# Kernel tuning notes

Measured on AMD Instinct MI355X. Metric: run time of the kernel, lower is better.

## Reference

```python
import jax, jax.numpy as jnp
import numpy as np

N_NODES = 100000
N_EDGES = 625000
D = 128
DEPTH = 2
BN_EPS = 1e-5


def setup_inputs() -> dict:
    key = jax.random.key(0)
    ks = jax.random.split(key, 8)
    x = jax.random.normal(ks[0], (N_NODES, D), dtype=jnp.float32)
    edge_index = jax.random.randint(ks[1], (2, N_EDGES), 0, N_NODES, dtype=jnp.int64)
    edge_weight = jax.random.uniform(ks[2], (N_EDGES,), dtype=jnp.float32)
    s = 1.0 / np.sqrt(D)
    W_lin = jax.random.uniform(ks[3], (DEPTH, D, D), jnp.float32, -s, s)
    W_gcn = jax.random.uniform(ks[4], (DEPTH, D, D), jnp.float32, -s, s)
    gamma = jnp.ones((DEPTH, D), jnp.float32)
    beta = jnp.zeros((DEPTH, D), jnp.float32)
    return {"x": x, "edge_index": edge_index, "edge_weight": edge_weight,
            "W_lin": W_lin, "W_gcn": W_gcn, "gamma": gamma, "beta": beta}


def reference(x, edge_index, edge_weight, W_lin, W_gcn, gamma, beta):
    n = x.shape[0]
    row, col = edge_index[0], edge_index[1]  # source, target
    # gcn_norm with add_self_loops=False: deg over targets, symmetric normalization
    deg = jax.ops.segment_sum(edge_weight, col, num_segments=n)
    dinv = jnp.where(deg > 0, jax.lax.rsqrt(deg), 0.0)
    norm = dinv[row] * edge_weight * dinv[col]  # [E]

    for i in range(DEPTH):
        hl = x @ W_lin[i].T                       # parallel linear branch
        hg = x @ W_gcn[i].T                       # GCNConv linear
        msg = norm[:, None] * hg[row]             # [E, D] messages
        hr = jax.ops.segment_sum(msg, col, num_segments=n)
        h = hl + hr
        # BatchNorm1d, training mode (batch statistics, biased variance)
        mu = jnp.mean(h, axis=0)
        var = jnp.mean((h - mu) ** 2, axis=0)
        h = (h - mu) * jax.lax.rsqrt(var + BN_EPS) * gamma[i] + beta[i]
        x = jnp.maximum(h, 0.0) if i != DEPTH - 1 else h
    return x
```

## Files before the change

kernel.cpp:

```cpp
#include <hip/hip_runtime.h>

#define NN 100000
#define NE 625000
#define DD 128
#define CAP 32
#define NREP 8

#define CONVB 12500
#define WPACKB 256
#define FILLBLK ((NE + 255) / 256)
#define GB ((NN + 63) / 64)

typedef __attribute__((ext_vector_type(8))) short bf16x8;
typedef __attribute__((ext_vector_type(4))) float f32x4;

static __device__ __forceinline__ unsigned short f2bf(float f) {
    union { float f; unsigned u; } v; v.f = f;
    unsigned u = v.u + 0x7fffu + ((v.u >> 16) & 1u);
    return (unsigned short)(u >> 16);
}
static __device__ __forceinline__ float bflo(unsigned u) { return __uint_as_float(u << 16); }
static __device__ __forceinline__ float bfhi(unsigned u) { return __uint_as_float(u & 0xffff0000u); }

__global__ __launch_bounds__(256) void k_pre(const float* __restrict__ x,
                                             unsigned* __restrict__ Xb2,
                                             const float* __restrict__ Wl,
                                             const float* __restrict__ Wg,
                                             unsigned short* __restrict__ wp,
                                             const int* __restrict__ row,
                                             const int* __restrict__ col,
                                             const float* __restrict__ w,
                                             int* __restrict__ cnt,
                                             int2* __restrict__ ebuf) {
    int b = blockIdx.x, t = threadIdx.x;
    if (b < CONVB) {
        size_t i = (size_t)b * 256 + t;
        size_t base = i * 4;
        float4 v = *(const float4*)&x[base];
        uint2 o;
        o.x = (unsigned)f2bf(v.x) | ((unsigned)f2bf(v.y) << 16);
        o.y = (unsigned)f2bf(v.z) | ((unsigned)f2bf(v.w) << 16);
        *(uint2*)&Xb2[i * 2] = o;
    } else if (b < CONVB + WPACKB) {
        int idx = (b - CONVB) * 256 + t;
        int l = idx >> 15;
        int rem = idx & 32767;
        int n = rem >> 8;
        int k = rem & 255;
        float v = (k < 128) ? Wl[(size_t)l * DD * DD + n * DD + k]
                            : Wg[(size_t)l * DD * DD + n * DD + (k - 128)];
        int wv = n >> 5;
        int tt = (n >> 4) & 1;
        int i  = n & 15;
        int ss = k >> 5;
        int q  = (k >> 3) & 3;
        int j  = k & 7;
        size_t off = ((size_t)((((l * 4 + wv) * 2 + tt) * 8 + ss)) * 64 + q * 16 + i) * 8 + j;
        wp[off] = f2bf(v);
    } else {
        int e = (b - CONVB - WPACKB) * 256 + t;
        if (e < NE) {
            int r = row[e], c = col[e];
            int pos = atomicAdd(&cnt[c], 1);
            if (pos < CAP) {
                int2 v; v.x = r; v.y = __float_as_int(w[e]);
                ebuf[(size_t)c * CAP + pos] = v;
            }
        }
    }
}

__global__ __launch_bounds__(256) void k_dinvb(const int* __restrict__ cnt,
                                               const int2* __restrict__ ebuf,
                                               float* __restrict__ dinv) {
    int t = threadIdx.x;
    int node = blockIdx.x * 32 + (t >> 3);
    int l = t & 7;
    int c = cnt[node]; if (c > CAP) c = CAP;
    float s = 0.f;
    for (int p = l; p < c; p += 8) s += __int_as_float(ebuf[(size_t)node * CAP + p].y);
    s += __shfl_down(s, 4, 8);
    s += __shfl_down(s, 2, 8);
    s += __shfl_down(s, 1, 8);
    if (l == 0) dinv[node] = (s > 0.f) ? rsqrtf(s) : 0.f;
}

template<int BN>
__global__ __launch_bounds__(256) void k_gatherP(const int* __restrict__ cnt,
                                                 const int2* __restrict__ ebuf,
                                                 const float* __restrict__ dinv,
                                                 const unsigned* __restrict__ X2,
                                                 const float* __restrict__ scale,
                                                 const float* __restrict__ shift,
                                                 unsigned* __restrict__ P2) {
    int t = threadIdx.x;
    int node = blockIdx.x * 4 + (t >> 6);
    int lane = t & 63;
    int c = cnt[node]; if (c > CAP) c = CAP;
    const int2* eb = ebuf + (size_t)node * CAP;
    float dn = dinv[node];
    float scx = 0.f, scy = 0.f, shx = 0.f, shy = 0.f;
    if (BN) {
        scx = scale[2 * lane]; scy = scale[2 * lane + 1];
        shx = shift[2 * lane]; shy = shift[2 * lane + 1];
    }
    float ax = 0.f, ay = 0.f;
    int p = 0;
    for (; p + 3 < c; p += 4) {
        int2 e0 = eb[p], e1 = eb[p + 1], e2 = eb[p + 2], e3 = eb[p + 3];
        float w0 = __int_as_float(e0.y) * dinv[e0.x] * dn;
        float w1 = __int_as_float(e1.y) * dinv[e1.x] * dn;
        float w2 = __int_as_float(e2.y) * dinv[e2.x] * dn;
        float w3 = __int_as_float(e3.y) * dinv[e3.x] * dn;
        unsigned u0 = X2[(size_t)e0.x * 64 + lane];
        unsigned u1 = X2[(size_t)e1.x * 64 + lane];
        unsigned u2 = X2[(size_t)e2.x * 64 + lane];
        unsigned u3 = X2[(size_t)e3.x * 64 + lane];
        float x0 = bflo(u0), y0 = bfhi(u0);
        float x1 = bflo(u1), y1 = bfhi(u1);
        float x2 = bflo(u2), y2 = bfhi(u2);
        float x3 = bflo(u3), y3 = bfhi(u3);
        if (BN) {
            x0 = fmaxf(x0 * scx + shx, 0.f); y0 = fmaxf(y0 * scy + shy, 0.f);
            x1 = fmaxf(x1 * scx + shx, 0.f); y1 = fmaxf(y1 * scy + shy, 0.f);
            x2 = fmaxf(x2 * scx + shx, 0.f); y2 = fmaxf(y2 * scy + shy, 0.f);
            x3 = fmaxf(x3 * scx + shx, 0.f); y3 = fmaxf(y3 * scy + shy, 0.f);
        }
        ax += w0 * x0 + w1 * x1 + w2 * x2 + w3 * x3;
        ay += w0 * y0 + w1 * y1 + w2 * y2 + w3 * y3;
    }
    for (; p < c; p++) {
        int2 e0 = eb[p];
        float w0 = __int_as_float(e0.y) * dinv[e0.x] * dn;
        unsigned u0 = X2[(size_t)e0.x * 64 + lane];
        float x0 = bflo(u0), y0 = bfhi(u0);
        if (BN) {
            x0 = fmaxf(x0 * scx + shx, 0.f); y0 = fmaxf(y0 * scy + shy, 0.f);
        }
        ax += w0 * x0;
        ay += w0 * y0;
    }
    P2[(size_t)node * 64 + lane] = (unsigned)f2bf(ax) | ((unsigned)f2bf(ay) << 16);
}

template<int LAYER>
__global__ __launch_bounds__(256) void k_gemm_s(const unsigned short* Xin,
                                                const unsigned short* P,
                                                const unsigned short* __restrict__ wp,
                                                const float* __restrict__ scale,
                                                const float* __restrict__ shift,
                                                unsigned short* Hout,
                                                float* __restrict__ stats) {
    __shared__ __align__(16) char smem[33792];
    unsigned short* sAv = (unsigned short*)smem;
    unsigned short* sBv = (unsigned short*)smem;
    float* red = (float*)(smem + 17408);

    const int t = threadIdx.x;
    const int wave = t >> 6;
    const int lane = t & 63;
    const int i16 = lane & 15;
    const int quad = lane >> 4;
    const int rowBase = blockIdx.x * 64;

    bf16x8 wf[2][8];
    #pragma unroll
    for (int tt = 0; tt < 2; tt++)
        #pragma unroll
        for (int ss = 0; ss < 8; ss++) {
            size_t off = ((size_t)(((wave * 2 + tt) * 8 + ss)) * 64 + quad * 16 + i16) * 8;
            wf[tt][ss] = *(const bf16x8*)&wp[off];
        }

    #pragma unroll
    for (int rep = 0; rep < 4; rep++) {
        int lin = rep * 2048 + t * 8;
        int r = lin >> 7, c = lin & 127;
        int rr = rowBase + r; if (rr >= NN) rr = NN - 1;
        uint4 u = *(const uint4*)&Xin[(size_t)rr * DD + c];
        if (LAYER == 1) {
            float4 sc0 = *(const float4*)&scale[c];
            float4 sc1 = *(const float4*)&scale[c + 4];
            float4 sh0 = *(const float4*)&shift[c];
            float4 sh1 = *(const float4*)&shift[c + 4];
            float v0 = fmaxf(bflo(u.x) * sc0.x + sh0.x, 0.f);
            float v1 = fmaxf(bfhi(u.x) * sc0.y + sh0.y, 0.f);
            float v2 = fmaxf(bflo(u.y) * sc0.z + sh0.z, 0.f);
            float v3 = fmaxf(bfhi(u.y) * sc0.w + sh0.w, 0.f);
            float v4 = fmaxf(bflo(u.z) * sc1.x + sh1.x, 0.f);
            float v5 = fmaxf(bfhi(u.z) * sc1.y + sh1.y, 0.f);
            float v6 = fmaxf(bflo(u.w) * sc1.z + sh1.z, 0.f);
            float v7 = fmaxf(bfhi(u.w) * sc1.w + sh1.w, 0.f);
            u.x = (unsigned)f2bf(v0) | ((unsigned)f2bf(v1) << 16);
            u.y = (unsigned)f2bf(v2) | ((unsigned)f2bf(v3) << 16);
            u.z = (unsigned)f2bf(v4) | ((unsigned)f2bf(v5) << 16);
            u.w = (unsigned)f2bf(v6) | ((unsigned)f2bf(v7) << 16);
        }
        *(uint4*)&sAv[r * 264 + c] = u;
    }
    #pragma unroll
    for (int rep = 0; rep < 4; rep++) {
        int lin = rep * 2048 + t * 8;
        int r = lin >> 7, c = lin & 127;
        int rr = rowBase + r; if (rr >= NN) rr = NN - 1;
        uint4 u = *(const uint4*)&P[(size_t)rr * DD + c];
        *(uint4*)&sAv[r * 264 + 128 + c] = u;
    }
    __syncthreads();

    f32x4 acc[4][2] = {{{0.f,0.f,0.f,0.f}}};
    #pragma unroll
    for (int ss = 0; ss < 8; ss++) {
        bf16x8 af[4];
        #pragma unroll
        for (int mt = 0; mt < 4; mt++)
            af[mt] = *(const bf16x8*)&sAv[(mt * 16 + i16) * 264 + ss * 32 + quad * 8];
        #pragma unroll
        for (int mt = 0; mt < 4; mt++)
            #pragma unroll
            for (int tt = 0; tt < 2; tt++)
                acc[mt][tt] = __builtin_amdgcn_mfma_f32_16x16x32_bf16(
                    af[mt], wf[tt][ss], acc[mt][tt], 0, 0, 0);
    }

    __syncthreads();
    #pragma unroll
    for (int mt = 0; mt < 4; mt++)
        #pragma unroll
        for (int r = 0; r < 4; r++) {
            int row = mt * 16 + quad * 4 + r;
            #pragma unroll
            for (int tt = 0; tt < 2; tt++)
                sBv[row * 136 + wave * 32 + tt * 16 + i16] = f2bf(acc[mt][tt][r]);
        }
    __syncthreads();

    float s[8] = {0.f,0.f,0.f,0.f,0.f,0.f,0.f,0.f};
    float q[8] = {0.f,0.f,0.f,0.f,0.f,0.f,0.f,0.f};
    const int cg = t & 15;
    #pragma unroll
    for (int it = 0; it < 4; it++) {
        int row = it * 16 + (t >> 4);
        int gr = rowBase + row;
        uint4 v = *(const uint4*)&sBv[row * 136 + cg * 8];
        float m = (gr < NN) ? 1.f : 0.f;
        if (gr < NN) *(uint4*)&Hout[(size_t)gr * DD + cg * 8] = v;
        float e0 = bflo(v.x) * m, e1 = bfhi(v.x) * m;
        float e2 = bflo(v.y) * m, e3 = bfhi(v.y) * m;
        float e4 = bflo(v.z) * m, e5 = bfhi(v.z) * m;
        float e6 = bflo(v.w) * m, e7 = bfhi(v.w) * m;
        s[0] += e0; q[0] += e0 * e0;  s[1] += e1; q[1] += e1 * e1;
        s[2] += e2; q[2] += e2 * e2;  s[3] += e3; q[3] += e3 * e3;
        s[4] += e4; q[4] += e4 * e4;  s[5] += e5; q[5] += e5 * e5;
        s[6] += e6; q[6] += e6 * e6;  s[7] += e7; q[7] += e7 * e7;
    }
    {
        int ro = t >> 4;
        #pragma unroll
        for (int j = 0; j < 8; j++) {
            red[(ro * 16 + cg) * 16 + j]     = s[j];
            red[(ro * 16 + cg) * 16 + 8 + j] = q[j];
        }
    }
    __syncthreads();
    {
        int colx = t & 127;
        int type = t >> 7;
        float tot = 0.f;
        #pragma unroll
        for (int ro = 0; ro < 16; ro++)
            tot += red[(ro * 16 + (colx >> 3)) * 16 + type * 8 + (colx & 7)];
        atomicAdd(&stats[(blockIdx.x & (NREP - 1)) * 256 + type * 128 + colx], tot);
    }
}

__global__ __launch_bounds__(128) void k_fold(const float* __restrict__ stats,
                                              const float* __restrict__ gamma,
                                              const float* __restrict__ beta,
                                              float* __restrict__ scale,
                                              float* __restrict__ shift) {
    int t = threadIdx.x;
    float sum = 0.f, sq = 0.f;
    #pragma unroll
    for (int rp = 0; rp < NREP; rp++) {
        sum += stats[rp * 256 + t];
        sq  += stats[rp * 256 + 128 + t];
    }
    float mu = sum * (1.0f / NN);
    float var = sq * (1.0f / NN) - mu * mu;
    float is = rsqrtf(var + 1e-5f);
    float sc = is * gamma[t];
    scale[t] = sc;
    shift[t] = beta[t] - mu * sc;
}

__global__ __launch_bounds__(256) void k_apply_out(const unsigned* __restrict__ H2,
                                                   const float* __restrict__ scale,
                                                   const float* __restrict__ shift,
                                                   float* __restrict__ out) {
    size_t i = (size_t)blockIdx.x * 256 + threadIdx.x;
    size_t base = i * 4;
    int c = (int)(base & 127);
    uint2 u = *(const uint2*)&H2[i * 2];
    float4 sc = *(const float4*)&scale[c];
    float4 sh = *(const float4*)&shift[c];
    float4 o;
    o.x = bflo(u.x) * sc.x + sh.x;
    o.y = bfhi(u.x) * sc.y + sh.y;
    o.z = bflo(u.y) * sc.z + sh.z;
    o.w = bfhi(u.y) * sc.w + sh.w;
    *(float4*)&out[base] = o;
}

extern "C" void kernel_launch(void* const* d_in, const int* in_sizes, int n_in,
                              void* d_out, int out_size, void* d_ws, size_t ws_size,
                              hipStream_t stream) {
    const float* x_in  = (const float*)d_in[0];
    const int*   ei    = (const int*)d_in[1];
    const float* ew    = (const float*)d_in[2];
    const float* Wl    = (const float*)d_in[3];
    const float* Wg    = (const float*)d_in[4];
    const float* gamma = (const float*)d_in[5];
    const float* beta  = (const float*)d_in[6];
    float* out = (float*)d_out;

    char* p = (char*)d_ws;
    unsigned short* bufA = (unsigned short*)p; p += (size_t)NN * DD * 2;
    unsigned short* bufB = (unsigned short*)p; p += (size_t)NN * DD * 2;
    int2* ebuf  = (int2*)p;  p += (size_t)NN * CAP * 8;
    int*   cnt    = (int*)p;   p += NN * 4;
    float* stats0 = (float*)p; p += NREP * 256 * 4;
    float* stats1 = (float*)p; p += NREP * 256 * 4;
    float* dinv   = (float*)p; p += 400000;
    float* scale0 = (float*)p; p += 512;
    float* shift0 = (float*)p; p += 512;
    float* scale1 = (float*)p; p += 512;
    float* shift1 = (float*)p; p += 512;
    unsigned short* wpack = (unsigned short*)p; p += 65536 * 2;

    const int* row = ei;
    const int* col = ei + NE;

    hipMemsetAsync(cnt, 0, NN * 4 + 2 * NREP * 256 * 4, stream);
    k_pre<<<CONVB + WPACKB + FILLBLK, 256, 0, stream>>>(
        x_in, (unsigned*)bufA, Wl, Wg, wpack, row, col, ew, cnt, ebuf);
    k_dinvb<<<NN / 32, 256, 0, stream>>>(cnt, ebuf, dinv);

    k_gatherP<0><<<NN / 4, 256, 0, stream>>>(cnt, ebuf, dinv, (const unsigned*)bufA,
                                             nullptr, nullptr, (unsigned*)bufB);
    k_gemm_s<0><<<GB, 256, 0, stream>>>(bufA, bufB, wpack, nullptr, nullptr, bufA, stats0);
    k_fold<<<1, 128, 0, stream>>>(stats0, gamma, beta, scale0, shift0);

    k_gatherP<1><<<NN / 4, 256, 0, stream>>>(cnt, ebuf, dinv, (const unsigned*)bufA,
                                             scale0, shift0, (unsigned*)bufB);
    k_gemm_s<1><<<GB, 256, 0, stream>>>(bufA, bufB, wpack + 32768, scale0, shift0, bufB, stats1);
    k_fold<<<1, 128, 0, stream>>>(stats1, gamma + DD, beta + DD, scale1, shift1);

    k_apply_out<<<NN * DD / 1024, 256, 0, stream>>>((const unsigned*)bufB, scale1, shift1, out);
}
```

Baseline: 293.2 us.

## Fuse neighbor gather into GEMM kernel and compute degree via atomics

The separate gather kernel is folded into the GEMM kernel: each wave aggregates 16 nodes' neighbor features directly into shared memory, so the intermediate P buffer is never written to or read back from global memory. Degree sums are now accumulated with float atomics during edge bucketing, which removes the dinv kernel, and dinv is recomputed with rsqrt inside the gather. Edge fill is vectorized four edges per thread, and GEMM input and output buffers are ping-ponged. The costs are per-edge rsqrt recomputation, doubled atomics in the fill stage, and fewer parallel blocks for the gather (GEMM grid of 1563 blocks instead of 25000), which may leave latency less well hidden.

```diff
diff --git a/kernel.cpp b/kernel.cpp
--- a/kernel.cpp
+++ b/kernel.cpp
@@ -8,7 +8,7 @@
 
 #define CONVB 12500
 #define WPACKB 256
-#define FILLBLK ((NE + 255) / 256)
+#define FILL4B ((NE / 4 + 255) / 256)
 #define GB ((NN + 63) / 64)
 
 typedef __attribute__((ext_vector_type(8))) short bf16x8;
@@ -30,19 +30,31 @@
                                              const int* __restrict__ row,
                                              const int* __restrict__ col,
                                              const float* __restrict__ w,
-                                             int* __restrict__ cnt,
+                                             int* __restrict__ cd,
                                              int2* __restrict__ ebuf) {
     int b = blockIdx.x, t = threadIdx.x;
-    if (b < CONVB) {
-        size_t i = (size_t)b * 256 + t;
-        size_t base = i * 4;
-        float4 v = *(const float4*)&x[base];
-        uint2 o;
-        o.x = (unsigned)f2bf(v.x) | ((unsigned)f2bf(v.y) << 16);
-        o.y = (unsigned)f2bf(v.z) | ((unsigned)f2bf(v.w) << 16);
-        *(uint2*)&Xb2[i * 2] = o;
-    } else if (b < CONVB + WPACKB) {
-        int idx = (b - CONVB) * 256 + t;
+    if (b < FILL4B) {
+        int id = b * 256 + t;
+        if (id < NE / 4) {
+            int e = id * 4;
+            int4 rr = *(const int4*)&row[e];
+            int4 cc = *(const int4*)&col[e];
+            float4 ww = *(const float4*)&w[e];
+            int p0 = atomicAdd(&cd[2 * cc.x], 1);
+            int p1 = atomicAdd(&cd[2 * cc.y], 1);
+            int p2 = atomicAdd(&cd[2 * cc.z], 1);
+            int p3 = atomicAdd(&cd[2 * cc.w], 1);
+            atomicAdd((float*)&cd[2 * cc.x + 1], ww.x);
+            atomicAdd((float*)&cd[2 * cc.y + 1], ww.y);
+            atomicAdd((float*)&cd[2 * cc.z + 1], ww.z);
+            atomicAdd((float*)&cd[2 * cc.w + 1], ww.w);
+            if (p0 < CAP) { int2 v; v.x = rr.x; v.y = __float_as_int(ww.x); ebuf[(size_t)cc.x * CAP + p0] = v; }
+            if (p1 < CAP) { int2 v; v.x = rr.y; v.y = __float_as_int(ww.y); ebuf[(size_t)cc.y * CAP + p1] = v; }
+            if (p2 < CAP) { int2 v; v.x = rr.z; v.y = __float_as_int(ww.z); ebuf[(size_t)cc.z * CAP + p2] = v; }
+            if (p3 < CAP) { int2 v; v.x = rr.w; v.y = __float_as_int(ww.w); ebuf[(size_t)cc.w * CAP + p3] = v; }
+        }
+    } else if (b < FILL4B + WPACKB) {
+        int idx = (b - FILL4B) * 256 + t;
         int l = idx >> 15;
         int rem = idx & 32767;
         int n = rem >> 8;
@@ -58,98 +70,24 @@
         size_t off = ((size_t)((((l * 4 + wv) * 2 + tt) * 8 + ss)) * 64 + q * 16 + i) * 8 + j;
         wp[off] = f2bf(v);
     } else {
-        int e = (b - CONVB - WPACKB) * 256 + t;
-        if (e < NE) {
-            int r = row[e], c = col[e];
-            int pos = atomicAdd(&cnt[c], 1);
-            if (pos < CAP) {
-                int2 v; v.x = r; v.y = __float_as_int(w[e]);
-                ebuf[(size_t)c * CAP + pos] = v;
-            }
-        }
-    }
-}
-
-__global__ __launch_bounds__(256) void k_dinvb(const int* __restrict__ cnt,
-                                               const int2* __restrict__ ebuf,
-                                               float* __restrict__ dinv) {
-    int t = threadIdx.x;
-    int node = blockIdx.x * 32 + (t >> 3);
-    int l = t & 7;
-    int c = cnt[node]; if (c > CAP) c = CAP;
-    float s = 0.f;
-    for (int p = l; p < c; p += 8) s += __int_as_float(ebuf[(size_t)node * CAP + p].y);
-    s += __shfl_down(s, 4, 8);
-    s += __shfl_down(s, 2, 8);
-    s += __shfl_down(s, 1, 8);
-    if (l == 0) dinv[node] = (s > 0.f) ? rsqrtf(s) : 0.f;
-}
-
-template<int BN>
-__global__ __launch_bounds__(256) void k_gatherP(const int* __restrict__ cnt,
-                                                 const int2* __restrict__ ebuf,
-                                                 const float* __restrict__ dinv,
-                                                 const unsigned* __restrict__ X2,
-                                                 const float* __restrict__ scale,
-                                                 const float* __restrict__ shift,
-                                                 unsigned* __restrict__ P2) {
-    int t = threadIdx.x;
-    int node = blockIdx.x * 4 + (t >> 6);
-    int lane = t & 63;
-    int c = cnt[node]; if (c > CAP) c = CAP;
-    const int2* eb = ebuf + (size_t)node * CAP;
-    float dn = dinv[node];
-    float scx = 0.f, scy = 0.f, shx = 0.f, shy = 0.f;
-    if (BN) {
-        scx = scale[2 * lane]; scy = scale[2 * lane + 1];
-        shx = shift[2 * lane]; shy = shift[2 * lane + 1];
-    }
-    float ax = 0.f, ay = 0.f;
-    int p = 0;
-    for (; p + 3 < c; p += 4) {
-        int2 e0 = eb[p], e1 = eb[p + 1], e2 = eb[p + 2], e3 = eb[p + 3];
-        float w0 = __int_as_float(e0.y) * dinv[e0.x] * dn;
-        float w1 = __int_as_float(e1.y) * dinv[e1.x] * dn;
-        float w2 = __int_as_float(e2.y) * dinv[e2.x] * dn;
-        float w3 = __int_as_float(e3.y) * dinv[e3.x] * dn;
-        unsigned u0 = X2[(size_t)e0.x * 64 + lane];
-        unsigned u1 = X2[(size_t)e1.x * 64 + lane];
-        unsigned u2 = X2[(size_t)e2.x * 64 + lane];
-        unsigned u3 = X2[(size_t)e3.x * 64 + lane];
-        float x0 = bflo(u0), y0 = bfhi(u0);
-        float x1 = bflo(u1), y1 = bfhi(u1);
-        float x2 = bflo(u2), y2 = bfhi(u2);
-        float x3 = bflo(u3), y3 = bfhi(u3);
-        if (BN) {
-            x0 = fmaxf(x0 * scx + shx, 0.f); y0 = fmaxf(y0 * scy + shy, 0.f);
-            x1 = fmaxf(x1 * scx + shx, 0.f); y1 = fmaxf(y1 * scy + shy, 0.f);
-            x2 = fmaxf(x2 * scx + shx, 0.f); y2 = fmaxf(y2 * scy + shy, 0.f);
-            x3 = fmaxf(x3 * scx + shx, 0.f); y3 = fmaxf(y3 * scy + shy, 0.f);
-        }
-        ax += w0 * x0 + w1 * x1 + w2 * x2 + w3 * x3;
-        ay += w0 * y0 + w1 * y1 + w2 * y2 + w3 * y3;
-    }
-    for (; p < c; p++) {
-        int2 e0 = eb[p];
-        float w0 = __int_as_float(e0.y) * dinv[e0.x] * dn;
-        unsigned u0 = X2[(size_t)e0.x * 64 + lane];
-        float x0 = bflo(u0), y0 = bfhi(u0);
-        if (BN) {
-            x0 = fmaxf(x0 * scx + shx, 0.f); y0 = fmaxf(y0 * scy + shy, 0.f);
-        }
-        ax += w0 * x0;
-        ay += w0 * y0;
-    }
-    P2[(size_t)node * 64 + lane] = (unsigned)f2bf(ax) | ((unsigned)f2bf(ay) << 16);
+        size_t i = (size_t)(b - FILL4B - WPACKB) * 256 + t;
+        size_t base = i * 4;
+        float4 v = *(const float4*)&x[base];
+        uint2 o;
+        o.x = (unsigned)f2bf(v.x) | ((unsigned)f2bf(v.y) << 16);
+        o.y = (unsigned)f2bf(v.z) | ((unsigned)f2bf(v.w) << 16);
+        *(uint2*)&Xb2[i * 2] = o;
+    }
 }
 
 template<int LAYER>
-__global__ __launch_bounds__(256) void k_gemm_s(const unsigned short* Xin,
-                                                const unsigned short* P,
+__global__ __launch_bounds__(256) void k_gemm_g(const unsigned short* __restrict__ Xin,
+                                                const int* __restrict__ cd,
+                                                const int2* __restrict__ ebuf,
                                                 const unsigned short* __restrict__ wp,
                                                 const float* __restrict__ scale,
                                                 const float* __restrict__ shift,
-                                                unsigned short* Hout,
+                                                unsigned short* __restrict__ Hout,
                                                 float* __restrict__ stats) {
     __shared__ __align__(16) char smem[33792];
     unsigned short* sAv = (unsigned short*)smem;
@@ -162,15 +100,7 @@
     const int i16 = lane & 15;
     const int quad = lane >> 4;
     const int rowBase = blockIdx.x * 64;
-
-    bf16x8 wf[2][8];
-    #pragma unroll
-    for (int tt = 0; tt < 2; tt++)
-        #pragma unroll
-        for (int ss = 0; ss < 8; ss++) {
-            size_t off = ((size_t)(((wave * 2 + tt) * 8 + ss)) * 64 + quad * 16 + i16) * 8;
-            wf[tt][ss] = *(const bf16x8*)&wp[off];
-        }
+    const unsigned* X2 = (const unsigned*)Xin;
 
     #pragma unroll
     for (int rep = 0; rep < 4; rep++) {
@@ -198,14 +128,77 @@
         }
         *(uint4*)&sAv[r * 264 + c] = u;
     }
-    #pragma unroll
-    for (int rep = 0; rep < 4; rep++) {
-        int lin = rep * 2048 + t * 8;
-        int r = lin >> 7, c = lin & 127;
-        int rr = rowBase + r; if (rr >= NN) rr = NN - 1;
-        uint4 u = *(const uint4*)&P[(size_t)rr * DD + c];
-        *(uint4*)&sAv[r * 264 + 128 + c] = u;
-    }
+
+    float scx = 0.f, scy = 0.f, shx = 0.f, shy = 0.f;
+    if (LAYER == 1) {
+        scx = scale[2 * lane]; scy = scale[2 * lane + 1];
+        shx = shift[2 * lane]; shy = shift[2 * lane + 1];
+    }
+    #pragma unroll 1
+    for (int ni = 0; ni < 16; ni++) {
+        int prow = wave * 16 + ni;
+        int node = rowBase + prow;
+        float ax = 0.f, ay = 0.f;
+        if (node < NN) {
+            int2 c2 = *(const int2*)&cd[2 * node];
+            int c = c2.x; if (c > CAP) c = CAP;
+            float dg = __int_as_float(c2.y);
+            float dn = (dg > 0.f) ? rsqrtf(dg) : 0.f;
+            const int2* eb = ebuf + (size_t)node * CAP;
+            int p = 0;
+            for (; p + 3 < c; p += 4) {
+                int2 e0 = eb[p], e1 = eb[p + 1], e2 = eb[p + 2], e3 = eb[p + 3];
+                float g0 = __int_as_float(cd[2 * e0.x + 1]);
+                float g1 = __int_as_float(cd[2 * e1.x + 1]);
+                float g2 = __int_as_float(cd[2 * e2.x + 1]);
+                float g3 = __int_as_float(cd[2 * e3.x + 1]);
+                float w0 = __int_as_float(e0.y) * ((g0 > 0.f) ? rsqrtf(g0) : 0.f);
+                float w1 = __int_as_float(e1.y) * ((g1 > 0.f) ? rsqrtf(g1) : 0.f);
+                float w2 = __int_as_float(e2.y) * ((g2 > 0.f) ? rsqrtf(g2) : 0.f);
+                float w3 = __int_as_float(e3.y) * ((g3 > 0.f) ? rsqrtf(g3) : 0.f);
+                unsigned u0 = X2[(size_t)e0.x * 64 + lane];
+                unsigned u1 = X2[(size_t)e1.x * 64 + lane];
+                unsigned u2 = X2[(size_t)e2.x * 64 + lane];
+                unsigned u3 = X2[(size_t)e3.x * 64 + lane];
+                float x0 = bflo(u0), y0 = bfhi(u0);
+                float x1 = bflo(u1), y1 = bfhi(u1);
+                float x2 = bflo(u2), y2 = bfhi(u2);
+                float x3 = bflo(u3), y3 = bfhi(u3);
+                if (LAYER == 1) {
+                    x0 = fmaxf(x0 * scx + shx, 0.f); y0 = fmaxf(y0 * scy + shy, 0.f);
+                    x1 = fmaxf(x1 * scx + shx, 0.f); y1 = fmaxf(y1 * scy + shy, 0.f);
+                    x2 = fmaxf(x2 * scx + shx, 0.f); y2 = fmaxf(y2 * scy + shy, 0.f);
+                    x3 = fmaxf(x3 * scx + shx, 0.f); y3 = fmaxf(y3 * scy + shy, 0.f);
+                }
+                ax += w0 * x0 + w1 * x1 + w2 * x2 + w3 * x3;
+                ay += w0 * y0 + w1 * y1 + w2 * y2 + w3 * y3;
+            }
+            for (; p < c; p++) {
+                int2 e0 = eb[p];
+                float g0 = __int_as_float(cd[2 * e0.x + 1]);
+                float w0 = __int_as_float(e0.y) * ((g0 > 0.f) ? rsqrtf(g0) : 0.f);
+                unsigned u0 = X2[(size_t)e0.x * 64 + lane];
+                float x0 = bflo(u0), y0 = bfhi(u0);
+                if (LAYER == 1) {
+                    x0 = fmaxf(x0 * scx + shx, 0.f); y0 = fmaxf(y0 * scy + shy, 0.f);
+                }
+                ax += w0 * x0;
+                ay += w0 * y0;
+            }
+            ax *= dn; ay *= dn;
+        }
+        *(unsigned*)&sAv[prow * 264 + 128 + 2 * lane] =
+            (unsigned)f2bf(ax) | ((unsigned)f2bf(ay) << 16);
+    }
+
+    bf16x8 wf[2][8];
+    #pragma unroll
+    for (int tt = 0; tt < 2; tt++)
+        #pragma unroll
+        for (int ss = 0; ss < 8; ss++) {
+            size_t off = ((size_t)(((wave * 2 + tt) * 8 + ss)) * 64 + quad * 16 + i16) * 8;
+            wf[tt][ss] = *(const bf16x8*)&wp[off];
+        }
     __syncthreads();
 
     f32x4 acc[4][2] = {{{0.f,0.f,0.f,0.f}}};
@@ -328,10 +321,9 @@
     unsigned short* bufA = (unsigned short*)p; p += (size_t)NN * DD * 2;
     unsigned short* bufB = (unsigned short*)p; p += (size_t)NN * DD * 2;
     int2* ebuf  = (int2*)p;  p += (size_t)NN * CAP * 8;
-    int*   cnt    = (int*)p;   p += NN * 4;
+    int*   cd     = (int*)p;   p += (size_t)NN * 8;
     float* stats0 = (float*)p; p += NREP * 256 * 4;
     float* stats1 = (float*)p; p += NREP * 256 * 4;
-    float* dinv   = (float*)p; p += 400000;
     float* scale0 = (float*)p; p += 512;
     float* shift0 = (float*)p; p += 512;
     float* scale1 = (float*)p; p += 512;
@@ -341,20 +333,17 @@
     const int* row = ei;
     const int* col = ei + NE;
 
-    hipMemsetAsync(cnt, 0, NN * 4 + 2 * NREP * 256 * 4, stream);
-    k_pre<<<CONVB + WPACKB + FILLBLK, 256, 0, stream>>>(
-        x_in, (unsigned*)bufA, Wl, Wg, wpack, row, col, ew, cnt, ebuf);
-    k_dinvb<<<NN / 32, 256, 0, stream>>>(cnt, ebuf, dinv);
-
-    k_gatherP<0><<<NN / 4, 256, 0, stream>>>(cnt, ebuf, dinv, (const unsigned*)bufA,
-                                             nullptr, nullptr, (unsigned*)bufB);
-    k_gemm_s<0><<<GB, 256, 0, stream>>>(bufA, bufB, wpack, nullptr, nullptr, bufA, stats0);
+    hipMemsetAsync(cd, 0, (size_t)NN * 8 + 2 * NREP * 256 * 4, stream);
+    k_pre<<<FILL4B + WPACKB + CONVB, 256, 0, stream>>>(
+        x_in, (unsigned*)bufA, Wl, Wg, wpack, row, col, ew, cd, ebuf);
+
+    k_gemm_g<0><<<GB, 256, 0, stream>>>(bufA, cd, ebuf, wpack,
+                                        nullptr, nullptr, bufB, stats0);
     k_fold<<<1, 128, 0, stream>>>(stats0, gamma, beta, scale0, shift0);
 
-    k_gatherP<1><<<NN / 4, 256, 0, stream>>>(cnt, ebuf, dinv, (const unsigned*)bufA,
-                                             scale0, shift0, (unsigned*)bufB);
-    k_gemm_s<1><<<GB, 256, 0, stream>>>(bufA, bufB, wpack + 32768, scale0, shift0, bufB, stats1);
+    k_gemm_g<1><<<GB, 256, 0, stream>>>(bufB, cd, ebuf, wpack + 32768,
+                                        scale0, shift0, bufA, stats1);
     k_fold<<<1, 128, 0, stream>>>(stats1, gamma + DD, beta + DD, scale1, shift1);
 
-    k_apply_out<<<NN * DD / 1024, 256, 0, stream>>>((const unsigned*)bufB, scale1, shift1, out);
-}
+    k_apply_out<<<NN * DD / 1024, 256, 0, stream>>>((const unsigned*)bufA, scale1, shift1, out);
+}
```

After: 417.3 us. +42.4%, slower.
